# Performance work log

Measured on AMD Instinct MI355X. Metric: run time of the kernel, lower is better.

Reference implementation:

```python
import jax, jax.numpy as jnp
from jax import lax
import numpy as np

B, DIM, H, W = 1, 1024, 24, 24
HEADS, GROUPS = 8, 4
TOPK_FRAC = 0.8
EPS = 1e-12


def setup_inputs() -> dict:
    key = jax.random.key(0)
    ks = jax.random.split(key, 5)
    t = GROUPS
    x = jax.random.normal(ks[0], (B, DIM, H, W), dtype=jnp.float32)
    # Conv3d(t, 3t, 1x1x1, bias=False): weight [3t, t]
    w_qkv = jax.random.normal(ks[1], (3 * t, t), dtype=jnp.float32) * 0.3
    # depthwise Conv3d(3t, 3t, (1,3,3), groups=3t): weight [3t, 3, 3]
    w_dw = jax.random.normal(ks[2], (3 * t, 3, 3), dtype=jnp.float32) * 0.2
    # temperature [1, heads, 1, 1]
    temperature = jnp.ones((1, HEADS, 1, 1), dtype=jnp.float32)
    # project_out Conv2d(dim, dim, 1): weight [dim, dim]
    w_proj = jax.random.normal(ks[3], (DIM, DIM), dtype=jnp.float32) * 0.02
    return {"x": x, "temperature": temperature, "w_qkv": w_qkv, "w_dw": w_dw, "w_proj": w_proj}


def _to_heads(u, b, t, cs, h, w):
    # [b, t, cs, h, w] -> [b, heads, ch, (h w t)]  (t fastest in flattened axis)
    ch = cs // HEADS
    u = u.reshape(b, t, HEADS, ch, h, w)
    u = u.transpose(0, 2, 3, 4, 5, 1)  # b, head, ch, h, w, t
    return u.reshape(b, HEADS, ch, h * w * t)


def reference(x, temperature, w_qkv, w_dw, w_proj):
    b, c, h, w = x.shape
    t = GROUPS
    cs = c // t
    xg = x.reshape(b, t, cs, h, w)
    # pointwise conv3d across group dim: [b, 3t, cs, h, w]
    qkv = jnp.einsum("btchw,st->bschw", xg, w_qkv)
    # depthwise (1,3,3) conv: fold cs into batch, 2D depthwise over (h, w)
    y = qkv.transpose(0, 2, 1, 3, 4).reshape(b * cs, 3 * t, h, w)
    kern = w_dw[:, None, :, :]  # [3t, 1, 3, 3]
    y = lax.conv_general_dilated(
        y, kern, window_strides=(1, 1), padding="SAME",
        dimension_numbers=("NCHW", "OIHW", "NCHW"), feature_group_count=3 * t)
    qkv = y.reshape(b, cs, 3 * t, h, w).transpose(0, 2, 1, 3, 4)
    q, k, v = qkv[:, :t], qkv[:, t:2 * t], qkv[:, 2 * t:]
    q = _to_heads(q, b, t, cs, h, w)
    k = _to_heads(k, b, t, cs, h, w)
    v = _to_heads(v, b, t, cs, h, w)
    # L2-normalize over token axis (dim=-1), torch eps semantics
    q = q / jnp.maximum(jnp.linalg.norm(q, axis=-1, keepdims=True), EPS)
    k = k / jnp.maximum(jnp.linalg.norm(k, axis=-1, keepdims=True), EPS)
    N = q.shape[-1]
    K = int(N * TOPK_FRAC)
    attn = jnp.einsum("bhcn,bhcm->bhnm", q, k) * temperature  # [b, heads, N, N]
    vals, idx = lax.top_k(attn, K)
    # scatter top-k values into a -inf matrix == where(mask>0, attn, -inf)
    bi = jnp.arange(b)[:, None, None, None]
    hi = jnp.arange(HEADS)[None, :, None, None]
    ni = jnp.arange(N)[None, None, :, None]
    masked = jnp.full_like(attn, -jnp.inf).at[bi, hi, ni, idx].set(vals)
    p = jax.nn.softmax(masked, axis=-1)
    out = jnp.einsum("bhnm,bhcm->bhcn", p, v)  # [b, heads, ch, N]
    ch = cs // HEADS
    out = out.reshape(b, HEADS, ch, h, w, t).transpose(0, 5, 1, 2, 3, 4).reshape(b, c, h, w)
    out = jnp.einsum("bchw,oc->bohw", out, w_proj)
    return x + out
```

## Files before the change

kernel.cpp:

```cpp
#include <hip/hip_runtime.h>
#include <math.h>

typedef unsigned int u32;
typedef unsigned long long u64;
typedef unsigned short u16;
typedef __attribute__((ext_vector_type(8))) short bf16x8;
typedef __attribute__((ext_vector_type(4))) float f32x4;

#define NHEADS 8
#define HH 24
#define WW 24
#define HW 576
#define CS 256
#define CHD 32
#define NN 2304
#define NGROUPS 4
#define TOPK 1843
#define DIM 1024
#define EPSN 1e-12f

__device__ __forceinline__ u32 fkey(float f) {
    u32 u = __float_as_uint(f);
    return u ^ ((u >> 31) ? 0xFFFFFFFFu : 0x80000000u);
}
__device__ __forceinline__ float fkey_inv(u32 k) {
    return __uint_as_float((k & 0x80000000u) ? (k ^ 0x80000000u) : ~k);
}
__device__ __forceinline__ u16 f2bf(float f) {
    u32 u = __float_as_uint(f);
    return (u16)((u + 0x7FFFu + ((u >> 16) & 1u)) >> 16);
}

__global__ __launch_bounds__(256) void qkv_conv_kernel(
    const float* __restrict__ x, const float* __restrict__ w_qkv,
    const float* __restrict__ w_dw,
    float* __restrict__ qb, float* __restrict__ kb, u16* __restrict__ vb16)
{
    __shared__ float xp[NGROUPS][26][26];
    __shared__ float wq[48];
    __shared__ float wd[108];
    int c = blockIdx.x;
    int tid = threadIdx.x;

    for (int i = tid; i < NGROUPS * 26 * 26; i += 256) ((float*)xp)[i] = 0.f;
    if (tid < 48) wq[tid] = w_qkv[tid];
    if (tid < 108) wd[tid] = w_dw[tid];
    __syncthreads();
    for (int i = tid; i < NGROUPS * HW; i += 256) {
        int t = i / HW, p = i % HW;
        int hh = p / WW, ww = p % WW;
        xp[t][hh + 1][ww + 1] = x[(size_t)(t * CS + c) * HW + p];
    }
    __syncthreads();

    int hd = c >> 5, ch = c & 31;
    for (int p = tid; p < HW; p += 256) {
        int hh = p / WW, ww = p % WW;
        float res[12];
        #pragma unroll
        for (int s = 0; s < 12; ++s) {
            float acc = 0.f;
            #pragma unroll
            for (int t = 0; t < NGROUPS; ++t) {
                float cv = 0.f;
                #pragma unroll
                for (int dh = 0; dh < 3; ++dh)
                    #pragma unroll
                    for (int dw = 0; dw < 3; ++dw)
                        cv += xp[t][hh + dh][ww + dw] * wd[s * 9 + dh * 3 + dw];
                acc += wq[s * 4 + t] * cv;
            }
            res[s] = acc;
        }
        #pragma unroll
        for (int tt = 0; tt < 4; ++tt) {
            int n = p * 4 + tt;
            size_t off = ((size_t)hd * CHD + ch) * NN + n;
            qb[off] = res[tt];
            kb[off] = res[4 + tt];
            vb16[off] = f2bf(res[8 + tt]);
        }
    }
}

__global__ __launch_bounds__(256) void norm_scale_kernel(
    const float* __restrict__ qb, const float* __restrict__ kb,
    float* __restrict__ scales)
{
    __shared__ float redf[5];
    int b = blockIdx.x;
    const float* rowp = ((b < 256) ? qb : kb) + (size_t)(b & 255) * NN;
    int tid = threadIdx.x;
    float ss = 0.f;
    for (int i = tid; i < NN; i += 256) { float v = rowp[i]; ss += v * v; }
    for (int off = 32; off > 0; off >>= 1) ss += __shfl_down(ss, off);
    int wid = tid >> 6, lane = tid & 63;
    if (lane == 0) redf[wid] = ss;
    __syncthreads();
    if (tid == 0)
        scales[b] = 1.f / fmaxf(sqrtf(redf[0] + redf[1] + redf[2] + redf[3]), EPSN);
}

__global__ __launch_bounds__(256) void transpose_cast_kernel(
    const float* __restrict__ qb, const float* __restrict__ kb,
    const float* __restrict__ scales,
    u16* __restrict__ Qt, u16* __restrict__ Kt)
{
    __shared__ float tile[32][33];
    int ntile = blockIdx.x;
    int h = blockIdx.y;
    int which = blockIdx.z;
    const float* src = which ? kb : qb;
    const float* scl = scales + which * 256;
    u16* dst = which ? Kt : Qt;
    int tid = threadIdx.x;
    int n0 = ntile * 32;
    #pragma unroll
    for (int cc = 0; cc < 32; cc += 8) {
        int c = cc + (tid >> 5);
        tile[c][tid & 31] = src[(size_t)(h * CHD + c) * NN + n0 + (tid & 31)]
                            * scl[h * CHD + c];
    }
    __syncthreads();
    int cgrp = tid & 7, nrow = tid >> 3;
    #pragma unroll
    for (int c0 = 0; c0 < 32; c0 += 16) {
        int c = c0 + cgrp * 2;
        u16 v0 = f2bf(tile[c][nrow]);
        u16 v1 = f2bf(tile[c + 1][nrow]);
        ushort2 v; v.x = v0; v.y = v1;
        *(ushort2*)(dst + ((size_t)h * NN + n0 + nrow) * CHD + c) = v;
    }
}

__global__ __launch_bounds__(256) void cast_wproj_kernel(
    const float* __restrict__ wp, u16* __restrict__ wpb)
{
    int i = blockIdx.x * 256 + threadIdx.x;
    float4 v = ((const float4*)wp)[i];
    ushort4 o;
    o.x = f2bf(v.x); o.y = f2bf(v.y); o.z = f2bf(v.z); o.w = f2bf(v.w);
    ((ushort4*)wpb)[i] = o;
}

__global__ __launch_bounds__(512, 2) void attn_fused2_kernel(
    const u16* __restrict__ Qt, const u16* __restrict__ Kt,
    const u16* __restrict__ Vb, const float* __restrict__ temp,
    u16* __restrict__ aoutT)
{
    __shared__ u32 hist[256][16];
    __shared__ u32 candK[16][64];
    __shared__ u32 candM[16][64];
    __shared__ u16 Pst[8][16][40];
    __shared__ u32 kminA[16], maxkA[16], shA[16], kloA[16], khiA[16],
                   remKA[16], stateA[16], TkeyA[16], candCnt[16];
    __shared__ int cutA[16];
    __shared__ float denomF[16];
    __shared__ u32 flagS;

    int tid = threadIdx.x;
    int lane = tid & 63;
    int w = tid >> 6;
    int q = lane >> 4;
    int cI = lane & 15;
    int h = blockIdx.x / 144;
    int n0 = (blockIdx.x % 144) * 16;

    for (int i = tid; i < 256 * 16; i += 512) ((u32*)hist)[i] = 0u;
    if (tid < 16) {
        kminA[tid] = 0xFFFFFFFFu; maxkA[tid] = 0u; candCnt[tid] = 0u;
        denomF[tid] = 0.f; stateA[tid] = 0u; cutA[tid] = NN - 1;
        remKA[tid] = TOPK; TkeyA[tid] = 0u;
    }
    __syncthreads();

    const u16* Qth = Qt + (size_t)h * NN * CHD;
    const u16* Kth = Kt + (size_t)h * NN * CHD;
    const u16* Vbh = Vb + (size_t)h * CHD * NN;
    float ts = temp[h];

    bf16x8 afrag = *(const bf16x8*)(Qth + (size_t)(n0 + cI) * CHD + q * 8);
    int mW = w * 288;
    const f32x4 zz = {0.f, 0.f, 0.f, 0.f};

    {
        u32 lmin[4], lmax[4];
        #pragma unroll
        for (int r = 0; r < 4; ++r) { lmin[r] = 0xFFFFFFFFu; lmax[r] = 0u; }
        #pragma unroll 2
        for (int t = 0; t < 18; ++t) {
            bf16x8 bfrag = *(const bf16x8*)(Kth + (size_t)(mW + t * 16 + cI) * CHD + q * 8);
            f32x4 a = __builtin_amdgcn_mfma_f32_16x16x32_bf16(afrag, bfrag, zz, 0, 0, 0);
            #pragma unroll
            for (int r = 0; r < 4; ++r) {
                u32 k = fkey(a[r] * ts);
                lmin[r] = min(lmin[r], k); lmax[r] = max(lmax[r], k);
            }
        }
        #pragma unroll
        for (int r = 0; r < 4; ++r) {
            #pragma unroll
            for (int mk = 1; mk < 16; mk <<= 1) {
                lmin[r] = min(lmin[r], (u32)__shfl_xor((int)lmin[r], mk));
                lmax[r] = max(lmax[r], (u32)__shfl_xor((int)lmax[r], mk));
            }
            if (cI == 0) {
                atomicMin(&kminA[4 * q + r], lmin[r]);
                atomicMax(&maxkA[4 * q + r], lmax[r]);
            }
        }
    }
    __syncthreads();
    if (tid < 16) {
        u32 range = maxkA[tid] - kminA[tid];
        shA[tid] = (range > 255u) ? (u32)(24 - __clz(range)) : 0u;
    }
    __syncthreads();

    {
        u32 km[4], sh[4];
        #pragma unroll
        for (int r = 0; r < 4; ++r) { km[r] = kminA[4 * q + r]; sh[r] = shA[4 * q + r]; }
        #pragma unroll 2
        for (int t = 0; t < 18; ++t) {
            bf16x8 bfrag = *(const bf16x8*)(Kth + (size_t)(mW + t * 16 + cI) * CHD + q * 8);
            f32x4 a = __builtin_amdgcn_mfma_f32_16x16x32_bf16(afrag, bfrag, zz, 0, 0, 0);
            #pragma unroll
            for (int r = 0; r < 4; ++r) {
                u32 k = fkey(a[r] * ts);
                atomicAdd(&hist[(k - km[r]) >> sh[r]][4 * q + r], 1u);
            }
        }
    }
    __syncthreads();

    #pragma unroll
    for (int rr = 0; rr < 2; ++rr) {
        int r = 2 * w + rr;
        u32 c0 = hist[lane * 4 + 0][r];
        u32 c1 = hist[lane * 4 + 1][r];
        u32 c2 = hist[lane * 4 + 2][r];
        u32 c3 = hist[lane * 4 + 3][r];
        u32 s3 = c3, s2 = c2 + s3, s1 = c1 + s2, s0 = c0 + s1;
        u32 suf = s0;
        #pragma unroll
        for (int off = 1; off < 64; off <<= 1) {
            u32 t2 = (u32)__shfl_down((int)suf, off);
            if (lane + off < 64) suf += t2;
        }
        u32 above_lane = suf - s0;
        u32 sArr[4] = {s0, s1, s2, s3};
        u32 cArr[4] = {c0, c1, c2, c3};
        u32 km = kminA[r], sh = shA[r];
        #pragma unroll
        for (int i = 0; i < 4; ++i) {
            u32 S = above_lane + sArr[i];
            u32 cb = cArr[i];
            if (S >= TOPK && S - cb < TOPK) {
                u32 b = lane * 4 + i;
                u32 klo = km + (b << sh);
                u64 khiL = (u64)km + ((u64)(b + 1) << sh) - 1ull;
                u32 khi = (khiL > 0xFFFFFFFFull) ? 0xFFFFFFFFu : (u32)khiL;
                kloA[r] = klo; khiA[r] = khi;
                remKA[r] = TOPK - (S - cb);
                if (cb <= 64u) stateA[r] = 1u;
                else if (klo == khi) { stateA[r] = 3u; TkeyA[r] = klo; }
                else stateA[r] = 0u;
            }
        }
    }
    __syncthreads();

    for (int round = 0; round < 4; ++round) {
        if (tid == 0) {
            u32 any = 0;
            for (int r = 0; r < 16; ++r) any |= (stateA[r] == 0u) ? 1u : 0u;
            flagS = any;
        }
        __syncthreads();
        if (!flagS) break;
        if (tid < 256) {
            for (int r = 0; r < 16; ++r)
                if (stateA[r] == 0u) hist[tid][r] = 0u;
        }
        __syncthreads();
        {
            u32 st[4], kl[4], kh[4], s2h[4];
            #pragma unroll
            for (int r = 0; r < 4; ++r) {
                int row = 4 * q + r;
                st[r] = stateA[row]; kl[r] = kloA[row]; kh[r] = khiA[row];
                u32 rg = kh[r] - kl[r];
                s2h[r] = (rg > 255u) ? (u32)(24 - __clz(rg)) : 0u;
            }
            #pragma unroll 2
            for (int t = 0; t < 18; ++t) {
                bf16x8 bfrag = *(const bf16x8*)(Kth + (size_t)(mW + t * 16 + cI) * CHD + q * 8);
                f32x4 a = __builtin_amdgcn_mfma_f32_16x16x32_bf16(afrag, bfrag, zz, 0, 0, 0);
                #pragma unroll
                for (int r = 0; r < 4; ++r) {
                    if (st[r] == 0u) {
                        u32 k = fkey(a[r] * ts);
                        if (k >= kl[r] && k <= kh[r])
                            atomicAdd(&hist[(k - kl[r]) >> s2h[r]][4 * q + r], 1u);
                    }
                }
            }
        }
        __syncthreads();
        #pragma unroll
        for (int rr = 0; rr < 2; ++rr) {
            int r = 2 * w + rr;
            if (stateA[r] != 0u) continue;
            u32 klo = kloA[r], khi = khiA[r];
            u32 rg = khi - klo;
            u32 sh = (rg > 255u) ? (u32)(24 - __clz(rg)) : 0u;
            u32 c0 = hist[lane * 4 + 0][r];
            u32 c1 = hist[lane * 4 + 1][r];
            u32 c2 = hist[lane * 4 + 2][r];
            u32 c3 = hist[lane * 4 + 3][r];
            u32 s3 = c3, s2 = c2 + s3, s1 = c1 + s2, s0 = c0 + s1;
            u32 suf = s0;
            #pragma unroll
            for (int off = 1; off < 64; off <<= 1) {
                u32 t2 = (u32)__shfl_down((int)suf, off);
                if (lane + off < 64) suf += t2;
            }
            u32 above_lane = suf - s0;
            u32 remK = remKA[r];
            u32 sArr[4] = {s0, s1, s2, s3};
            u32 cArr[4] = {c0, c1, c2, c3};
            #pragma unroll
            for (int i = 0; i < 4; ++i) {
                u32 S = above_lane + sArr[i];
                u32 cb = cArr[i];
                if (S >= remK && S - cb < remK) {
                    u32 b = lane * 4 + i;
                    u32 nlo = klo + (b << sh);
                    u64 nhiL = (u64)klo + ((u64)(b + 1) << sh) - 1ull;
                    u32 nhi = (nhiL > (u64)khi) ? khi : (u32)nhiL;
                    kloA[r] = nlo; khiA[r] = nhi;
                    remKA[r] = remK - (S - cb);
                    if (cb <= 64u) stateA[r] = 1u;
                    else if (nlo == nhi) { stateA[r] = 3u; TkeyA[r] = nlo; }
                    else stateA[r] = 0u;
                }
            }
        }
        __syncthreads();
    }
    if (tid < 16 && stateA[tid] == 0u) {
        TkeyA[tid] = kloA[tid]; stateA[tid] = 3u;
    }
    __syncthreads();

    {
        u32 st[4], kl[4], kh[4];
        #pragma unroll
        for (int r = 0; r < 4; ++r) {
            int row = 4 * q + r;
            st[r] = stateA[row]; kl[r] = kloA[row]; kh[r] = khiA[row];
        }
        #pragma unroll 2
        for (int t = 0; t < 18; ++t) {
            bf16x8 bfrag = *(const bf16x8*)(Kth + (size_t)(mW + t * 16 + cI) * CHD + q * 8);
            f32x4 a = __builtin_amdgcn_mfma_f32_16x16x32_bf16(afrag, bfrag, zz, 0, 0, 0);
            int m = mW + t * 16 + cI;
            #pragma unroll
            for (int r = 0; r < 4; ++r) {
                if (st[r] == 1u) {
                    u32 k = fkey(a[r] * ts);
                    if (k >= kl[r] && k <= kh[r]) {
                        int row = 4 * q + r;
                        u32 pos = atomicAdd(&candCnt[row], 1u);
                        if (pos < 64u) { candK[row][pos] = k; candM[row][pos] = (u32)m; }
                    }
                }
            }
        }
    }
    __syncthreads();

    #pragma unroll
    for (int rr = 0; rr < 2; ++rr) {
        int r = 2 * w + rr;
        if (stateA[r] == 1u) {
            u32 cnt = min(candCnt[r], 64u);
            u32 remK = remKA[r];
            u32 myk = 0u, mym = 0u;
            if (lane < (int)cnt) { myk = candK[r][lane]; mym = candM[r][lane]; }
            u32 gtr = 0;
            for (u32 i = 0; i < cnt; ++i) {
                u32 ki = candK[r][i], mi = candM[r][i];
                gtr += (ki > myk || (ki == myk && mi < mym)) ? 1u : 0u;
            }
            if (lane < (int)cnt && gtr == remK - 1u) {
                TkeyA[r] = myk; cutA[r] = (int)mym;
            }
        }
    }
    __syncthreads();

    {
        float maxf[4], ls[4];
        u32 Tr[4]; int cutr[4];
        #pragma unroll
        for (int r = 0; r < 4; ++r) {
            int row = 4 * q + r;
            maxf[r] = fkey_inv(maxkA[row]);
            Tr[r] = TkeyA[row];
            cutr[r] = cutA[row];
            ls[r] = 0.f;
        }
        f32x4 acc0 = {0.f, 0.f, 0.f, 0.f};
        f32x4 acc1 = {0.f, 0.f, 0.f, 0.f};
        for (int j = 0; j < 9; ++j) {
            int mb = mW + j * 32;
            bf16x8 b0 = *(const bf16x8*)(Kth + (size_t)(mb + cI) * CHD + q * 8);
            bf16x8 b1 = *(const bf16x8*)(Kth + (size_t)(mb + 16 + cI) * CHD + q * 8);
            f32x4 a0 = __builtin_amdgcn_mfma_f32_16x16x32_bf16(afrag, b0, zz, 0, 0, 0);
            f32x4 a1 = __builtin_amdgcn_mfma_f32_16x16x32_bf16(afrag, b1, zz, 0, 0, 0);
            #pragma unroll
            for (int r = 0; r < 4; ++r) {
                {
                    float s = a0[r] * ts;
                    u32 k = fkey(s);
                    int m = mb + cI;
                    bool inc = (k > Tr[r]) || (k == Tr[r] && m <= cutr[r]);
                    float p = inc ? __expf(s - maxf[r]) : 0.f;
                    ls[r] += p;
                    Pst[w][4 * q + r][cI] = f2bf(p);
                }
                {
                    float s = a1[r] * ts;
                    u32 k = fkey(s);
                    int m = mb + 16 + cI;
                    bool inc = (k > Tr[r]) || (k == Tr[r] && m <= cutr[r]);
                    float p = inc ? __expf(s - maxf[r]) : 0.f;
                    ls[r] += p;
                    Pst[w][4 * q + r][16 + cI] = f2bf(p);
                }
            }
            bf16x8 pf = *(const bf16x8*)&Pst[w][cI][q * 8];
            bf16x8 v0 = *(const bf16x8*)(Vbh + (size_t)cI * NN + mb + q * 8);
            bf16x8 v1 = *(const bf16x8*)(Vbh + (size_t)(16 + cI) * NN + mb + q * 8);
            acc0 = __builtin_amdgcn_mfma_f32_16x16x32_bf16(v0, pf, acc0, 0, 0, 0);
            acc1 = __builtin_amdgcn_mfma_f32_16x16x32_bf16(v1, pf, acc1, 0, 0, 0);
        }
        #pragma unroll
        for (int r = 0; r < 4; ++r) {
            #pragma unroll
            for (int mk = 1; mk < 16; mk <<= 1)
                ls[r] += __shfl_xor(ls[r], mk);
            if (cI == 0) atomicAdd(&denomF[4 * q + r], ls[r]);
        }
        __syncthreads();
        float* red = (float*)hist;
        #pragma unroll
        for (int r = 0; r < 4; ++r) {
            red[((size_t)w * 32 + (4 * q + r)) * 16 + cI] = acc0[r];
            red[((size_t)w * 32 + 16 + (4 * q + r)) * 16 + cI] = acc1[r];
        }
    }
    __syncthreads();

    {
        const float* red = (const float*)hist;
        int c = tid >> 4, n = tid & 15;
        float s = 0.f;
        #pragma unroll
        for (int w2 = 0; w2 < 8; ++w2) s += red[((size_t)w2 * 32 + c) * 16 + n];
        s /= denomF[n];
        int ng = n0 + n;
        int t = ng & 3, p = ng >> 2;
        aoutT[(size_t)p * DIM + t * CS + h * CHD + c] = f2bf(s);
    }
}

__global__ __launch_bounds__(256) void proj_mfma_kernel(
    const u16* __restrict__ aoutT, const u16* __restrict__ wpb,
    const float* __restrict__ x, float* __restrict__ out)
{
    int tid = threadIdx.x, lane = tid & 63, w = tid >> 6;
    int q = lane >> 4, cI = lane & 15;
    int p0 = blockIdx.x * 16;
    int o0 = blockIdx.y * 64 + w * 16;
    f32x4 acc = {0.f, 0.f, 0.f, 0.f};
    const u16* arow = wpb + (size_t)(o0 + cI) * DIM + q * 8;
    const u16* brow = aoutT + (size_t)(p0 + cI) * DIM + q * 8;
    #pragma unroll 8
    for (int k = 0; k < DIM; k += 32) {
        bf16x8 af = *(const bf16x8*)(arow + k);
        bf16x8 bf = *(const bf16x8*)(brow + k);
        acc = __builtin_amdgcn_mfma_f32_16x16x32_bf16(af, bf, acc, 0, 0, 0);
    }
    #pragma unroll
    for (int r = 0; r < 4; ++r) {
        int o = o0 + 4 * q + r, p = p0 + cI;
        out[(size_t)o * HW + p] = x[(size_t)o * HW + p] + acc[r];
    }
}

extern "C" void kernel_launch(void* const* d_in, const int* in_sizes, int n_in,
                              void* d_out, int out_size, void* d_ws, size_t ws_size,
                              hipStream_t stream)
{
    const float* x     = (const float*)d_in[0];
    const float* temp  = (const float*)d_in[1];
    const float* w_qkv = (const float*)d_in[2];
    const float* w_dw  = (const float*)d_in[3];
    const float* wproj = (const float*)d_in[4];
    float* out = (float*)d_out;

    const size_t T = (size_t)NHEADS * CHD * NN;
    char* ws = (char*)d_ws;
    float* qb    = (float*)(ws);
    float* kb    = (float*)(ws + 4 * T);
    u16*   Qt    = (u16*)(ws + 8 * T);
    u16*   Kt    = (u16*)(ws + 10 * T);
    u16*   Vb    = (u16*)(ws + 12 * T);
    u16*   aoutT = (u16*)(ws + 14 * T);
    u16*   wpb   = (u16*)(ws + 16 * T);
    float* scales= (float*)(ws + 16 * T + (size_t)DIM * DIM * 2);

    qkv_conv_kernel<<<256, 256, 0, stream>>>(x, w_qkv, w_dw, qb, kb, Vb);
    norm_scale_kernel<<<512, 256, 0, stream>>>(qb, kb, scales);
    transpose_cast_kernel<<<dim3(72, 8, 2), 256, 0, stream>>>(qb, kb, scales, Qt, Kt);
    cast_wproj_kernel<<<DIM * DIM / 4 / 256, 256, 0, stream>>>(wproj, wpb);
    attn_fused2_kernel<<<NHEADS * 144, 512, 0, stream>>>(Qt, Kt, Vb, temp, aoutT);
    proj_mfma_kernel<<<dim3(36, 16), 256, 0, stream>>>(aoutT, wpb, x, out);
}
```

Baseline: 181.3 us.

## Cache attention score keys in registers across top-k passes instead of recomputing

Each wave now computes its 18x4 block of QK^T score keys once, keeps them in a 72-element register array, and reuses them for the histogram, refinement, candidate-gathering and softmax/PV passes. This removes the repeated K-fragment loads and MFMAs of the earlier passes. The histogram is also transposed to [row][bin] with a padded stride of 257 to change the LDS bank pattern of the atomics. The cost is much higher register pressure under launch_bounds(512,2), which could cause spills. Recovering scores via fkey_inv is exact, since the key mapping is bijective.

```diff
diff --git a/kernel.cpp b/kernel.cpp
--- a/kernel.cpp
+++ b/kernel.cpp
@@ -143,12 +143,12 @@
     ((ushort4*)wpb)[i] = o;
 }
 
-__global__ __launch_bounds__(512, 2) void attn_fused2_kernel(
+__global__ __launch_bounds__(512, 2) void attn_reg_kernel(
     const u16* __restrict__ Qt, const u16* __restrict__ Kt,
     const u16* __restrict__ Vb, const float* __restrict__ temp,
     u16* __restrict__ aoutT)
 {
-    __shared__ u32 hist[256][16];
+    __shared__ u32 hist[16][257];
     __shared__ u32 candK[16][64];
     __shared__ u32 candM[16][64];
     __shared__ u16 Pst[8][16][40];
@@ -166,7 +166,7 @@
     int h = blockIdx.x / 144;
     int n0 = (blockIdx.x % 144) * 16;
 
-    for (int i = tid; i < 256 * 16; i += 512) ((u32*)hist)[i] = 0u;
+    for (int i = tid; i < 16 * 257; i += 512) ((u32*)hist)[i] = 0u;
     if (tid < 16) {
         kminA[tid] = 0xFFFFFFFFu; maxkA[tid] = 0u; candCnt[tid] = 0u;
         denomF[tid] = 0.f; stateA[tid] = 0u; cutA[tid] = NN - 1;
@@ -183,17 +183,19 @@
     int mW = w * 288;
     const f32x4 zz = {0.f, 0.f, 0.f, 0.f};
 
+    u32 kk[18][4];
     {
         u32 lmin[4], lmax[4];
         #pragma unroll
         for (int r = 0; r < 4; ++r) { lmin[r] = 0xFFFFFFFFu; lmax[r] = 0u; }
-        #pragma unroll 2
+        #pragma unroll
         for (int t = 0; t < 18; ++t) {
             bf16x8 bfrag = *(const bf16x8*)(Kth + (size_t)(mW + t * 16 + cI) * CHD + q * 8);
             f32x4 a = __builtin_amdgcn_mfma_f32_16x16x32_bf16(afrag, bfrag, zz, 0, 0, 0);
             #pragma unroll
             for (int r = 0; r < 4; ++r) {
                 u32 k = fkey(a[r] * ts);
+                kk[t][r] = k;
                 lmin[r] = min(lmin[r], k); lmax[r] = max(lmax[r], k);
             }
         }
@@ -221,15 +223,11 @@
         u32 km[4], sh[4];
         #pragma unroll
         for (int r = 0; r < 4; ++r) { km[r] = kminA[4 * q + r]; sh[r] = shA[4 * q + r]; }
-        #pragma unroll 2
+        #pragma unroll
         for (int t = 0; t < 18; ++t) {
-            bf16x8 bfrag = *(const bf16x8*)(Kth + (size_t)(mW + t * 16 + cI) * CHD + q * 8);
-            f32x4 a = __builtin_amdgcn_mfma_f32_16x16x32_bf16(afrag, bfrag, zz, 0, 0, 0);
-            #pragma unroll
-            for (int r = 0; r < 4; ++r) {
-                u32 k = fkey(a[r] * ts);
-                atomicAdd(&hist[(k - km[r]) >> sh[r]][4 * q + r], 1u);
-            }
+            #pragma unroll
+            for (int r = 0; r < 4; ++r)
+                atomicAdd(&hist[4 * q + r][(kk[t][r] - km[r]) >> sh[r]], 1u);
         }
     }
     __syncthreads();
@@ -237,10 +235,10 @@
     #pragma unroll
     for (int rr = 0; rr < 2; ++rr) {
         int r = 2 * w + rr;
-        u32 c0 = hist[lane * 4 + 0][r];
-        u32 c1 = hist[lane * 4 + 1][r];
-        u32 c2 = hist[lane * 4 + 2][r];
-        u32 c3 = hist[lane * 4 + 3][r];
+        u32 c0 = hist[r][lane * 4 + 0];
+        u32 c1 = hist[r][lane * 4 + 1];
+        u32 c2 = hist[r][lane * 4 + 2];
+        u32 c3 = hist[r][lane * 4 + 3];
         u32 s3 = c3, s2 = c2 + s3, s1 = c1 + s2, s0 = c0 + s1;
         u32 suf = s0;
         #pragma unroll
@@ -279,9 +277,9 @@
         }
         __syncthreads();
         if (!flagS) break;
-        if (tid < 256) {
+        if (tid < 257) {
             for (int r = 0; r < 16; ++r)
-                if (stateA[r] == 0u) hist[tid][r] = 0u;
+                if (stateA[r] == 0u) hist[r][tid] = 0u;
         }
         __syncthreads();
         {
@@ -293,16 +291,14 @@
                 u32 rg = kh[r] - kl[r];
                 s2h[r] = (rg > 255u) ? (u32)(24 - __clz(rg)) : 0u;
             }
-            #pragma unroll 2
+            #pragma unroll
             for (int t = 0; t < 18; ++t) {
-                bf16x8 bfrag = *(const bf16x8*)(Kth + (size_t)(mW + t * 16 + cI) * CHD + q * 8);
-                f32x4 a = __builtin_amdgcn_mfma_f32_16x16x32_bf16(afrag, bfrag, zz, 0, 0, 0);
                 #pragma unroll
                 for (int r = 0; r < 4; ++r) {
                     if (st[r] == 0u) {
-                        u32 k = fkey(a[r] * ts);
+                        u32 k = kk[t][r];
                         if (k >= kl[r] && k <= kh[r])
-                            atomicAdd(&hist[(k - kl[r]) >> s2h[r]][4 * q + r], 1u);
+                            atomicAdd(&hist[4 * q + r][(k - kl[r]) >> s2h[r]], 1u);
                     }
                 }
             }
@@ -315,10 +311,10 @@
             u32 klo = kloA[r], khi = khiA[r];
             u32 rg = khi - klo;
             u32 sh = (rg > 255u) ? (u32)(24 - __clz(rg)) : 0u;
-            u32 c0 = hist[lane * 4 + 0][r];
-            u32 c1 = hist[lane * 4 + 1][r];
-            u32 c2 = hist[lane * 4 + 2][r];
-            u32 c3 = hist[lane * 4 + 3][r];
+            u32 c0 = hist[r][lane * 4 + 0];
+            u32 c1 = hist[r][lane * 4 + 1];
+            u32 c2 = hist[r][lane * 4 + 2];
+            u32 c3 = hist[r][lane * 4 + 3];
             u32 s3 = c3, s2 = c2 + s3, s1 = c1 + s2, s0 = c0 + s1;
             u32 suf = s0;
             #pragma unroll
@@ -361,15 +357,13 @@
             int row = 4 * q + r;
             st[r] = stateA[row]; kl[r] = kloA[row]; kh[r] = khiA[row];
         }
-        #pragma unroll 2
+        #pragma unroll
         for (int t = 0; t < 18; ++t) {
-            bf16x8 bfrag = *(const bf16x8*)(Kth + (size_t)(mW + t * 16 + cI) * CHD + q * 8);
-            f32x4 a = __builtin_amdgcn_mfma_f32_16x16x32_bf16(afrag, bfrag, zz, 0, 0, 0);
             int m = mW + t * 16 + cI;
             #pragma unroll
             for (int r = 0; r < 4; ++r) {
                 if (st[r] == 1u) {
-                    u32 k = fkey(a[r] * ts);
+                    u32 k = kk[t][r];
                     if (k >= kl[r] && k <= kh[r]) {
                         int row = 4 * q + r;
                         u32 pos = atomicAdd(&candCnt[row], 1u);
@@ -414,29 +408,24 @@
         }
         f32x4 acc0 = {0.f, 0.f, 0.f, 0.f};
         f32x4 acc1 = {0.f, 0.f, 0.f, 0.f};
+        #pragma unroll
         for (int j = 0; j < 9; ++j) {
             int mb = mW + j * 32;
-            bf16x8 b0 = *(const bf16x8*)(Kth + (size_t)(mb + cI) * CHD + q * 8);
-            bf16x8 b1 = *(const bf16x8*)(Kth + (size_t)(mb + 16 + cI) * CHD + q * 8);
-            f32x4 a0 = __builtin_amdgcn_mfma_f32_16x16x32_bf16(afrag, b0, zz, 0, 0, 0);
-            f32x4 a1 = __builtin_amdgcn_mfma_f32_16x16x32_bf16(afrag, b1, zz, 0, 0, 0);
             #pragma unroll
             for (int r = 0; r < 4; ++r) {
                 {
-                    float s = a0[r] * ts;
-                    u32 k = fkey(s);
+                    u32 k = kk[2 * j][r];
                     int m = mb + cI;
                     bool inc = (k > Tr[r]) || (k == Tr[r] && m <= cutr[r]);
-                    float p = inc ? __expf(s - maxf[r]) : 0.f;
+                    float p = inc ? __expf(fkey_inv(k) - maxf[r]) : 0.f;
                     ls[r] += p;
                     Pst[w][4 * q + r][cI] = f2bf(p);
                 }
                 {
-                    float s = a1[r] * ts;
-                    u32 k = fkey(s);
+                    u32 k = kk[2 * j + 1][r];
                     int m = mb + 16 + cI;
                     bool inc = (k > Tr[r]) || (k == Tr[r] && m <= cutr[r]);
-                    float p = inc ? __expf(s - maxf[r]) : 0.f;
+                    float p = inc ? __expf(fkey_inv(k) - maxf[r]) : 0.f;
                     ls[r] += p;
                     Pst[w][4 * q + r][16 + cI] = f2bf(p);
                 }
@@ -527,6 +516,6 @@
     norm_scale_kernel<<<512, 256, 0, stream>>>(qb, kb, scales);
     transpose_cast_kernel<<<dim3(72, 8, 2), 256, 0, stream>>>(qb, kb, scales, Qt, Kt);
     cast_wproj_kernel<<<DIM * DIM / 4 / 256, 256, 0, stream>>>(wproj, wpb);
-    attn_fused2_kernel<<<NHEADS * 144, 512, 0, stream>>>(Qt, Kt, Vb, temp, aoutT);
+    attn_reg_kernel<<<NHEADS * 144, 512, 0, stream>>>(Qt, Kt, Vb, temp, aoutT);
     proj_mfma_kernel<<<dim3(36, 16), 256, 0, stream>>>(aoutT, wpb, x, out);
 }
```

New measurement: 191.3 us. +5.6%, slower.

## Run top-k attention per 16-query tile in a single wave instead of eight

Applied to the files above, without the earlier changes.

Replaces the 512-thread attention block, which split keys across eight waves, with a single-wave block that scans all keys per 16-query tile. It removes cross-wave atomics, the shared-memory reduction of partial outputs, and most block barriers. The histogram is narrowed to 128 bins in a padded row-major layout, and candidate ranking uses shuffles. The cost is fewer resident waves and longer serial loops per block, which may reduce latency hiding.

```diff
diff --git a/kernel.cpp b/kernel.cpp
--- a/kernel.cpp
+++ b/kernel.cpp
@@ -143,54 +143,44 @@
     ((ushort4*)wpb)[i] = o;
 }
 
-__global__ __launch_bounds__(512, 2) void attn_fused2_kernel(
+__global__ __launch_bounds__(64) void attn_wave_kernel(
     const u16* __restrict__ Qt, const u16* __restrict__ Kt,
     const u16* __restrict__ Vb, const float* __restrict__ temp,
     u16* __restrict__ aoutT)
 {
-    __shared__ u32 hist[256][16];
+    __shared__ u32 hist[16][129];
     __shared__ u32 candK[16][64];
     __shared__ u32 candM[16][64];
-    __shared__ u16 Pst[8][16][40];
-    __shared__ u32 kminA[16], maxkA[16], shA[16], kloA[16], khiA[16],
-                   remKA[16], stateA[16], TkeyA[16], candCnt[16];
-    __shared__ int cutA[16];
-    __shared__ float denomF[16];
-    __shared__ u32 flagS;
-
-    int tid = threadIdx.x;
-    int lane = tid & 63;
-    int w = tid >> 6;
-    int q = lane >> 4;
-    int cI = lane & 15;
+    __shared__ u16 Pst[16][40];
+    __shared__ u32 rowMinS[16], rowMaxS[16], kloS[16], khiS[16],
+                   remKS[16], cntS[16], stateS[16], TkeyS[16], candCntS[16];
+    __shared__ int cutS[16];
+    __shared__ float denomS[16];
+
+    int lane = threadIdx.x;
+    int q = lane >> 4, cI = lane & 15;
     int h = blockIdx.x / 144;
     int n0 = (blockIdx.x % 144) * 16;
 
-    for (int i = tid; i < 256 * 16; i += 512) ((u32*)hist)[i] = 0u;
-    if (tid < 16) {
-        kminA[tid] = 0xFFFFFFFFu; maxkA[tid] = 0u; candCnt[tid] = 0u;
-        denomF[tid] = 0.f; stateA[tid] = 0u; cutA[tid] = NN - 1;
-        remKA[tid] = TOPK; TkeyA[tid] = 0u;
-    }
-    __syncthreads();
+    for (int i = lane; i < 16 * 129; i += 64) ((u32*)hist)[i] = 0u;
+    if (lane < 16) {
+        candCntS[lane] = 0u; stateS[lane] = 0u; cutS[lane] = NN - 1;
+        remKS[lane] = TOPK; TkeyS[lane] = 0u;
+    }
 
     const u16* Qth = Qt + (size_t)h * NN * CHD;
     const u16* Kth = Kt + (size_t)h * NN * CHD;
     const u16* Vbh = Vb + (size_t)h * CHD * NN;
     float ts = temp[h];
-
     bf16x8 afrag = *(const bf16x8*)(Qth + (size_t)(n0 + cI) * CHD + q * 8);
-    int mW = w * 288;
     const f32x4 zz = {0.f, 0.f, 0.f, 0.f};
 
     {
-        u32 lmin[4], lmax[4];
-        #pragma unroll
-        for (int r = 0; r < 4; ++r) { lmin[r] = 0xFFFFFFFFu; lmax[r] = 0u; }
-        #pragma unroll 2
-        for (int t = 0; t < 18; ++t) {
-            bf16x8 bfrag = *(const bf16x8*)(Kth + (size_t)(mW + t * 16 + cI) * CHD + q * 8);
-            f32x4 a = __builtin_amdgcn_mfma_f32_16x16x32_bf16(afrag, bfrag, zz, 0, 0, 0);
+        u32 lmin[4] = {~0u, ~0u, ~0u, ~0u}, lmax[4] = {0u, 0u, 0u, 0u};
+        #pragma unroll 4
+        for (int t = 0; t < 144; ++t) {
+            bf16x8 bf = *(const bf16x8*)(Kth + (size_t)(t * 16 + cI) * CHD + q * 8);
+            f32x4 a = __builtin_amdgcn_mfma_f32_16x16x32_bf16(afrag, bf, zz, 0, 0, 0);
             #pragma unroll
             for (int r = 0; r < 4; ++r) {
                 u32 k = fkey(a[r] * ts);
@@ -204,175 +194,161 @@
                 lmin[r] = min(lmin[r], (u32)__shfl_xor((int)lmin[r], mk));
                 lmax[r] = max(lmax[r], (u32)__shfl_xor((int)lmax[r], mk));
             }
-            if (cI == 0) {
-                atomicMin(&kminA[4 * q + r], lmin[r]);
-                atomicMax(&maxkA[4 * q + r], lmax[r]);
-            }
-        }
-    }
-    __syncthreads();
-    if (tid < 16) {
-        u32 range = maxkA[tid] - kminA[tid];
-        shA[tid] = (range > 255u) ? (u32)(24 - __clz(range)) : 0u;
+        }
+        if (cI == 0) {
+            #pragma unroll
+            for (int r = 0; r < 4; ++r) {
+                rowMinS[4 * q + r] = lmin[r];
+                rowMaxS[4 * q + r] = lmax[r];
+            }
+        }
     }
     __syncthreads();
 
     {
         u32 km[4], sh[4];
         #pragma unroll
-        for (int r = 0; r < 4; ++r) { km[r] = kminA[4 * q + r]; sh[r] = shA[4 * q + r]; }
+        for (int r = 0; r < 4; ++r) {
+            u32 mn = rowMinS[4 * q + r];
+            u32 rg = rowMaxS[4 * q + r] - mn;
+            km[r] = mn;
+            sh[r] = (rg > 127u) ? (u32)(25 - __clz(rg)) : 0u;
+        }
         #pragma unroll 2
-        for (int t = 0; t < 18; ++t) {
-            bf16x8 bfrag = *(const bf16x8*)(Kth + (size_t)(mW + t * 16 + cI) * CHD + q * 8);
-            f32x4 a = __builtin_amdgcn_mfma_f32_16x16x32_bf16(afrag, bfrag, zz, 0, 0, 0);
+        for (int t = 0; t < 144; ++t) {
+            bf16x8 bf = *(const bf16x8*)(Kth + (size_t)(t * 16 + cI) * CHD + q * 8);
+            f32x4 a = __builtin_amdgcn_mfma_f32_16x16x32_bf16(afrag, bf, zz, 0, 0, 0);
             #pragma unroll
             for (int r = 0; r < 4; ++r) {
                 u32 k = fkey(a[r] * ts);
-                atomicAdd(&hist[(k - km[r]) >> sh[r]][4 * q + r], 1u);
-            }
-        }
-    }
-    __syncthreads();
-
-    #pragma unroll
-    for (int rr = 0; rr < 2; ++rr) {
-        int r = 2 * w + rr;
-        u32 c0 = hist[lane * 4 + 0][r];
-        u32 c1 = hist[lane * 4 + 1][r];
-        u32 c2 = hist[lane * 4 + 2][r];
-        u32 c3 = hist[lane * 4 + 3][r];
-        u32 s3 = c3, s2 = c2 + s3, s1 = c1 + s2, s0 = c0 + s1;
+                atomicAdd(&hist[4 * q + r][(k - km[r]) >> sh[r]], 1u);
+            }
+        }
+    }
+    __syncthreads();
+
+    for (int row = 0; row < 16; ++row) {
+        u32 c0 = hist[row][lane * 2], c1 = hist[row][lane * 2 + 1];
+        u32 s1 = c1, s0 = c0 + c1;
         u32 suf = s0;
         #pragma unroll
         for (int off = 1; off < 64; off <<= 1) {
             u32 t2 = (u32)__shfl_down((int)suf, off);
             if (lane + off < 64) suf += t2;
         }
-        u32 above_lane = suf - s0;
-        u32 sArr[4] = {s0, s1, s2, s3};
-        u32 cArr[4] = {c0, c1, c2, c3};
-        u32 km = kminA[r], sh = shA[r];
-        #pragma unroll
-        for (int i = 0; i < 4; ++i) {
-            u32 S = above_lane + sArr[i];
-            u32 cb = cArr[i];
+        u32 above = suf - s0;
+        u32 mn = rowMinS[row];
+        u32 rg = rowMaxS[row] - mn;
+        u32 shr = (rg > 127u) ? (u32)(25 - __clz(rg)) : 0u;
+        u32 sArr[2] = {above + s0, above + s1};
+        u32 cArr[2] = {c0, c1};
+        #pragma unroll
+        for (int i = 0; i < 2; ++i) {
+            u32 S = sArr[i], cb = cArr[i];
             if (S >= TOPK && S - cb < TOPK) {
-                u32 b = lane * 4 + i;
-                u32 klo = km + (b << sh);
-                u64 khiL = (u64)km + ((u64)(b + 1) << sh) - 1ull;
+                u32 b = lane * 2 + i;
+                u32 klo = mn + (b << shr);
+                u64 khiL = (u64)mn + ((u64)(b + 1) << shr) - 1ull;
                 u32 khi = (khiL > 0xFFFFFFFFull) ? 0xFFFFFFFFu : (u32)khiL;
-                kloA[r] = klo; khiA[r] = khi;
-                remKA[r] = TOPK - (S - cb);
-                if (cb <= 64u) stateA[r] = 1u;
-                else if (klo == khi) { stateA[r] = 3u; TkeyA[r] = klo; }
-                else stateA[r] = 0u;
-            }
-        }
-    }
-    __syncthreads();
-
-    for (int round = 0; round < 4; ++round) {
-        if (tid == 0) {
-            u32 any = 0;
-            for (int r = 0; r < 16; ++r) any |= (stateA[r] == 0u) ? 1u : 0u;
-            flagS = any;
-        }
-        __syncthreads();
-        if (!flagS) break;
-        if (tid < 256) {
-            for (int r = 0; r < 16; ++r)
-                if (stateA[r] == 0u) hist[tid][r] = 0u;
-        }
+                kloS[row] = klo; khiS[row] = khi;
+                remKS[row] = TOPK - (S - cb); cntS[row] = cb;
+                if (cb <= 64u) stateS[row] = 1u;
+                else if (klo == khi) { stateS[row] = 3u; TkeyS[row] = klo; }
+                else stateS[row] = 0u;
+            }
+        }
+    }
+    __syncthreads();
+
+    for (int round = 0; round < 5; ++round) {
+        u64 bal = __ballot(lane < 16 && stateS[lane] == 0u);
+        if (bal == 0ull) break;
+        for (int row = 0; row < 16; ++row)
+            if (stateS[row] == 0u) { if (lane < 64) { for (int i = lane; i < 129; i += 64) hist[row][i] = 0u; } }
         __syncthreads();
         {
-            u32 st[4], kl[4], kh[4], s2h[4];
+            u32 st2[4], kl2[4], sh2[4], kh2[4];
             #pragma unroll
             for (int r = 0; r < 4; ++r) {
                 int row = 4 * q + r;
-                st[r] = stateA[row]; kl[r] = kloA[row]; kh[r] = khiA[row];
-                u32 rg = kh[r] - kl[r];
-                s2h[r] = (rg > 255u) ? (u32)(24 - __clz(rg)) : 0u;
+                st2[r] = stateS[row]; kl2[r] = kloS[row]; kh2[r] = khiS[row];
+                u32 rg = kh2[r] - kl2[r];
+                sh2[r] = (rg > 127u) ? (u32)(25 - __clz(rg)) : 0u;
             }
             #pragma unroll 2
-            for (int t = 0; t < 18; ++t) {
-                bf16x8 bfrag = *(const bf16x8*)(Kth + (size_t)(mW + t * 16 + cI) * CHD + q * 8);
-                f32x4 a = __builtin_amdgcn_mfma_f32_16x16x32_bf16(afrag, bfrag, zz, 0, 0, 0);
+            for (int t = 0; t < 144; ++t) {
+                bf16x8 bf = *(const bf16x8*)(Kth + (size_t)(t * 16 + cI) * CHD + q * 8);
+                f32x4 a = __builtin_amdgcn_mfma_f32_16x16x32_bf16(afrag, bf, zz, 0, 0, 0);
                 #pragma unroll
                 for (int r = 0; r < 4; ++r) {
-                    if (st[r] == 0u) {
+                    if (st2[r] == 0u) {
                         u32 k = fkey(a[r] * ts);
-                        if (k >= kl[r] && k <= kh[r])
-                            atomicAdd(&hist[(k - kl[r]) >> s2h[r]][4 * q + r], 1u);
+                        if (k >= kl2[r] && k <= kh2[r])
+                            atomicAdd(&hist[4 * q + r][(k - kl2[r]) >> sh2[r]], 1u);
                     }
                 }
             }
         }
         __syncthreads();
-        #pragma unroll
-        for (int rr = 0; rr < 2; ++rr) {
-            int r = 2 * w + rr;
-            if (stateA[r] != 0u) continue;
-            u32 klo = kloA[r], khi = khiA[r];
-            u32 rg = khi - klo;
-            u32 sh = (rg > 255u) ? (u32)(24 - __clz(rg)) : 0u;
-            u32 c0 = hist[lane * 4 + 0][r];
-            u32 c1 = hist[lane * 4 + 1][r];
-            u32 c2 = hist[lane * 4 + 2][r];
-            u32 c3 = hist[lane * 4 + 3][r];
-            u32 s3 = c3, s2 = c2 + s3, s1 = c1 + s2, s0 = c0 + s1;
+        for (int row = 0; row < 16; ++row) {
+            if (stateS[row] != 0u) continue;
+            u32 base = kloS[row], khiR = khiS[row];
+            u32 rg = khiR - base;
+            u32 shr = (rg > 127u) ? (u32)(25 - __clz(rg)) : 0u;
+            u32 remK = remKS[row];
+            u32 c0 = hist[row][lane * 2], c1 = hist[row][lane * 2 + 1];
+            u32 s1 = c1, s0 = c0 + c1;
             u32 suf = s0;
             #pragma unroll
             for (int off = 1; off < 64; off <<= 1) {
                 u32 t2 = (u32)__shfl_down((int)suf, off);
                 if (lane + off < 64) suf += t2;
             }
-            u32 above_lane = suf - s0;
-            u32 remK = remKA[r];
-            u32 sArr[4] = {s0, s1, s2, s3};
-            u32 cArr[4] = {c0, c1, c2, c3};
-            #pragma unroll
-            for (int i = 0; i < 4; ++i) {
-                u32 S = above_lane + sArr[i];
-                u32 cb = cArr[i];
+            u32 above = suf - s0;
+            u32 sArr[2] = {above + s0, above + s1};
+            u32 cArr[2] = {c0, c1};
+            #pragma unroll
+            for (int i = 0; i < 2; ++i) {
+                u32 S = sArr[i], cb = cArr[i];
                 if (S >= remK && S - cb < remK) {
-                    u32 b = lane * 4 + i;
-                    u32 nlo = klo + (b << sh);
-                    u64 nhiL = (u64)klo + ((u64)(b + 1) << sh) - 1ull;
-                    u32 nhi = (nhiL > (u64)khi) ? khi : (u32)nhiL;
-                    kloA[r] = nlo; khiA[r] = nhi;
-                    remKA[r] = remK - (S - cb);
-                    if (cb <= 64u) stateA[r] = 1u;
-                    else if (nlo == nhi) { stateA[r] = 3u; TkeyA[r] = nlo; }
-                    else stateA[r] = 0u;
+                    u32 b = lane * 2 + i;
+                    u32 nlo = base + (b << shr);
+                    u64 nhiL = (u64)base + ((u64)(b + 1) << shr) - 1ull;
+                    u32 nhi = (nhiL > (u64)khiR) ? khiR : (u32)nhiL;
+                    kloS[row] = nlo; khiS[row] = nhi;
+                    remKS[row] = remK - (S - cb); cntS[row] = cb;
+                    if (cb <= 64u) stateS[row] = 1u;
+                    else if (nlo == nhi) { stateS[row] = 3u; TkeyS[row] = nlo; }
+                    else stateS[row] = 0u;
                 }
             }
         }
         __syncthreads();
     }
-    if (tid < 16 && stateA[tid] == 0u) {
-        TkeyA[tid] = kloA[tid]; stateA[tid] = 3u;
+    if (lane < 16 && stateS[lane] == 0u) {
+        TkeyS[lane] = kloS[lane]; stateS[lane] = 3u;
     }
     __syncthreads();
 
     {
-        u32 st[4], kl[4], kh[4];
+        u32 st3[4], kl3[4], kh3[4];
         #pragma unroll
         for (int r = 0; r < 4; ++r) {
             int row = 4 * q + r;
-            st[r] = stateA[row]; kl[r] = kloA[row]; kh[r] = khiA[row];
+            st3[r] = stateS[row]; kl3[r] = kloS[row]; kh3[r] = khiS[row];
         }
         #pragma unroll 2
-        for (int t = 0; t < 18; ++t) {
-            bf16x8 bfrag = *(const bf16x8*)(Kth + (size_t)(mW + t * 16 + cI) * CHD + q * 8);
-            f32x4 a = __builtin_amdgcn_mfma_f32_16x16x32_bf16(afrag, bfrag, zz, 0, 0, 0);
-            int m = mW + t * 16 + cI;
+        for (int t = 0; t < 144; ++t) {
+            bf16x8 bf = *(const bf16x8*)(Kth + (size_t)(t * 16 + cI) * CHD + q * 8);
+            f32x4 a = __builtin_amdgcn_mfma_f32_16x16x32_bf16(afrag, bf, zz, 0, 0, 0);
+            int m = t * 16 + cI;
             #pragma unroll
             for (int r = 0; r < 4; ++r) {
-                if (st[r] == 1u) {
+                if (st3[r] == 1u) {
                     u32 k = fkey(a[r] * ts);
-                    if (k >= kl[r] && k <= kh[r]) {
+                    if (k >= kl3[r] && k <= kh3[r]) {
                         int row = 4 * q + r;
-                        u32 pos = atomicAdd(&candCnt[row], 1u);
+                        u32 pos = atomicAdd(&candCntS[row], 1u);
                         if (pos < 64u) { candK[row][pos] = k; candM[row][pos] = (u32)m; }
                     }
                 }
@@ -381,41 +357,39 @@
     }
     __syncthreads();
 
+    for (int row = 0; row < 16; ++row) {
+        if (stateS[row] != 1u) continue;
+        u32 cnt = min(cntS[row], 64u);
+        u32 remK = remKS[row];
+        u32 myk = 0u, mym = 0xFFFFFFFFu;
+        if (lane < (int)cnt) { myk = candK[row][lane]; mym = candM[row][lane]; }
+        u32 gtr = 0;
+        for (u32 i = 0; i < cnt; ++i) {
+            u32 ki = (u32)__shfl((int)myk, (int)i);
+            u32 mi = (u32)__shfl((int)mym, (int)i);
+            gtr += (ki > myk || (ki == myk && mi < mym)) ? 1u : 0u;
+        }
+        if (lane < (int)cnt && gtr == remK - 1u) {
+            TkeyS[row] = myk; cutS[row] = (int)mym;
+        }
+    }
+    __syncthreads();
+
+    float maxf[4], ls[4];
+    u32 Tr[4]; int cutr[4];
     #pragma unroll
-    for (int rr = 0; rr < 2; ++rr) {
-        int r = 2 * w + rr;
-        if (stateA[r] == 1u) {
-            u32 cnt = min(candCnt[r], 64u);
-            u32 remK = remKA[r];
-            u32 myk = 0u, mym = 0u;
-            if (lane < (int)cnt) { myk = candK[r][lane]; mym = candM[r][lane]; }
-            u32 gtr = 0;
-            for (u32 i = 0; i < cnt; ++i) {
-                u32 ki = candK[r][i], mi = candM[r][i];
-                gtr += (ki > myk || (ki == myk && mi < mym)) ? 1u : 0u;
-            }
-            if (lane < (int)cnt && gtr == remK - 1u) {
-                TkeyA[r] = myk; cutA[r] = (int)mym;
-            }
-        }
-    }
-    __syncthreads();
-
-    {
-        float maxf[4], ls[4];
-        u32 Tr[4]; int cutr[4];
-        #pragma unroll
-        for (int r = 0; r < 4; ++r) {
-            int row = 4 * q + r;
-            maxf[r] = fkey_inv(maxkA[row]);
-            Tr[r] = TkeyA[row];
-            cutr[r] = cutA[row];
-            ls[r] = 0.f;
-        }
-        f32x4 acc0 = {0.f, 0.f, 0.f, 0.f};
-        f32x4 acc1 = {0.f, 0.f, 0.f, 0.f};
-        for (int j = 0; j < 9; ++j) {
-            int mb = mW + j * 32;
+    for (int r = 0; r < 4; ++r) {
+        int row = 4 * q + r;
+        maxf[r] = fkey_inv(rowMaxS[row]);
+        Tr[r] = TkeyS[row];
+        cutr[r] = cutS[row];
+        ls[r] = 0.f;
+    }
+    f32x4 accA0 = zz, accA1 = zz, accB0 = zz, accB1 = zz;
+    for (int jj = 0; jj < 36; ++jj) {
+        #pragma unroll
+        for (int half = 0; half < 2; ++half) {
+            int mb = jj * 64 + half * 32;
             bf16x8 b0 = *(const bf16x8*)(Kth + (size_t)(mb + cI) * CHD + q * 8);
             bf16x8 b1 = *(const bf16x8*)(Kth + (size_t)(mb + 16 + cI) * CHD + q * 8);
             f32x4 a0 = __builtin_amdgcn_mfma_f32_16x16x32_bf16(afrag, b0, zz, 0, 0, 0);
@@ -429,7 +403,7 @@
                     bool inc = (k > Tr[r]) || (k == Tr[r] && m <= cutr[r]);
                     float p = inc ? __expf(s - maxf[r]) : 0.f;
                     ls[r] += p;
-                    Pst[w][4 * q + r][cI] = f2bf(p);
+                    Pst[4 * q + r][cI] = f2bf(p);
                 }
                 {
                     float s = a1[r] * ts;
@@ -438,42 +412,43 @@
                     bool inc = (k > Tr[r]) || (k == Tr[r] && m <= cutr[r]);
                     float p = inc ? __expf(s - maxf[r]) : 0.f;
                     ls[r] += p;
-                    Pst[w][4 * q + r][16 + cI] = f2bf(p);
+                    Pst[4 * q + r][16 + cI] = f2bf(p);
                 }
             }
-            bf16x8 pf = *(const bf16x8*)&Pst[w][cI][q * 8];
+            bf16x8 pf = *(const bf16x8*)&Pst[cI][q * 8];
             bf16x8 v0 = *(const bf16x8*)(Vbh + (size_t)cI * NN + mb + q * 8);
             bf16x8 v1 = *(const bf16x8*)(Vbh + (size_t)(16 + cI) * NN + mb + q * 8);
-            acc0 = __builtin_amdgcn_mfma_f32_16x16x32_bf16(v0, pf, acc0, 0, 0, 0);
-            acc1 = __builtin_amdgcn_mfma_f32_16x16x32_bf16(v1, pf, acc1, 0, 0, 0);
-        }
+            if (half == 0) {
+                accA0 = __builtin_amdgcn_mfma_f32_16x16x32_bf16(v0, pf, accA0, 0, 0, 0);
+                accA1 = __builtin_amdgcn_mfma_f32_16x16x32_bf16(v1, pf, accA1, 0, 0, 0);
+            } else {
+                accB0 = __builtin_amdgcn_mfma_f32_16x16x32_bf16(v0, pf, accB0, 0, 0, 0);
+                accB1 = __builtin_amdgcn_mfma_f32_16x16x32_bf16(v1, pf, accB1, 0, 0, 0);
+            }
+        }
+    }
+    #pragma unroll
+    for (int r = 0; r < 4; ++r) {
+        #pragma unroll
+        for (int mk = 1; mk < 16; mk <<= 1)
+            ls[r] += __shfl_xor(ls[r], mk);
+    }
+    if (cI == 0) {
+        #pragma unroll
+        for (int r = 0; r < 4; ++r) denomS[4 * q + r] = ls[r];
+    }
+    __syncthreads();
+
+    {
+        float dnv = 1.f / denomS[cI];
+        int ng = n0 + cI;
+        int tt = ng & 3, pp = ng >> 2;
+        size_t base = (size_t)pp * DIM + tt * CS + h * CHD;
         #pragma unroll
         for (int r = 0; r < 4; ++r) {
-            #pragma unroll
-            for (int mk = 1; mk < 16; mk <<= 1)
-                ls[r] += __shfl_xor(ls[r], mk);
-            if (cI == 0) atomicAdd(&denomF[4 * q + r], ls[r]);
-        }
-        __syncthreads();
-        float* red = (float*)hist;
-        #pragma unroll
-        for (int r = 0; r < 4; ++r) {
-            red[((size_t)w * 32 + (4 * q + r)) * 16 + cI] = acc0[r];
-            red[((size_t)w * 32 + 16 + (4 * q + r)) * 16 + cI] = acc1[r];
-        }
-    }
-    __syncthreads();
-
-    {
-        const float* red = (const float*)hist;
-        int c = tid >> 4, n = tid & 15;
-        float s = 0.f;
-        #pragma unroll
-        for (int w2 = 0; w2 < 8; ++w2) s += red[((size_t)w2 * 32 + c) * 16 + n];
-        s /= denomF[n];
-        int ng = n0 + n;
-        int t = ng & 3, p = ng >> 2;
-        aoutT[(size_t)p * DIM + t * CS + h * CHD + c] = f2bf(s);
+            aoutT[base + 4 * q + r]      = f2bf((accA0[r] + accB0[r]) * dnv);
+            aoutT[base + 16 + 4 * q + r] = f2bf((accA1[r] + accB1[r]) * dnv);
+        }
     }
 }
 
@@ -527,6 +502,6 @@
     norm_scale_kernel<<<512, 256, 0, stream>>>(qb, kb, scales);
     transpose_cast_kernel<<<dim3(72, 8, 2), 256, 0, stream>>>(qb, kb, scales, Qt, Kt);
     cast_wproj_kernel<<<DIM * DIM / 4 / 256, 256, 0, stream>>>(wproj, wpb);
-    attn_fused2_kernel<<<NHEADS * 144, 512, 0, stream>>>(Qt, Kt, Vb, temp, aoutT);
+    attn_wave_kernel<<<NHEADS * 144, 64, 0, stream>>>(Qt, Kt, Vb, temp, aoutT);
     proj_mfma_kernel<<<dim3(36, 16), 256, 0, stream>>>(aoutT, wpb, x, out);
 }
```

Result: slower. 293.9 us (+62.2%).
